# Kernel tuning notes

Hardware: AMD Instinct MI355X
Metric: run time of the kernel (lower is better)

Reference implementation:

```python
import jax, jax.numpy as jnp
import numpy as np

D = 1024  # in_features
H = 16    # head_num

def setup_inputs() -> dict:
    key = jax.random.key(0)
    ks = jax.random.split(key, 11)
    S, B = 2048, 2
    scale = 1.0 / np.sqrt(D)
    inp = {
        'q': jax.random.normal(ks[0], (S, B, D), jnp.float32),
        'k': jax.random.normal(ks[1], (S, B, D), jnp.float32),
        'v': jax.random.normal(ks[2], (S, B, D), jnp.float32),
        'Wq': jax.random.normal(ks[3], (D, D), jnp.float32) * scale,
        'Wk': jax.random.normal(ks[4], (D, D), jnp.float32) * scale,
        'Wv': jax.random.normal(ks[5], (D, D), jnp.float32) * scale,
        'Wo': jax.random.normal(ks[6], (D, D), jnp.float32) * scale,
        'bq': jax.random.normal(ks[7], (D,), jnp.float32) * 0.01,
        'bk': jax.random.normal(ks[8], (D,), jnp.float32) * 0.01,
        'bv': jax.random.normal(ks[9], (D,), jnp.float32) * 0.01,
        'bo': jax.random.normal(ks[10], (D,), jnp.float32) * 0.01,
    }
    return inp

def reference(q, k, v, Wq, Wk, Wv, Wo, bq, bk, bv, bo):
    # q,k,v: (S, B, D) -> (B, S, D)
    q = jnp.transpose(q, (1, 0, 2))
    k = jnp.transpose(k, (1, 0, 2))
    v = jnp.transpose(v, (1, 0, 2))
    # linear + ReLU (torch Linear: x @ W.T + b)
    qh = jax.nn.relu(q @ Wq.T + bq)
    kh = jax.nn.relu(k @ Wk.T + bk)
    vh = jax.nn.relu(v @ Wv.T + bv)
    B, S, _ = qh.shape
    hd = D // H
    # (B, S, H, hd) -> (B, H, S, hd)
    qh = qh.reshape(B, S, H, hd).transpose(0, 2, 1, 3)
    kh = kh.reshape(B, S, H, hd).transpose(0, 2, 1, 3)
    vh = vh.reshape(B, S, H, hd).transpose(0, 2, 1, 3)
    scores = jnp.einsum('bhsd,bhtd->bhst', qh, kh) / np.sqrt(hd).astype(np.float32)
    attn = jax.nn.softmax(scores, axis=-1)
    y = jnp.einsum('bhst,bhtd->bhsd', attn, vh)  # (B, H, S, hd)
    y = y.transpose(0, 2, 1, 3).reshape(B, S, D)
    y = jax.nn.relu(y @ Wo.T + bo)
    return jnp.transpose(y, (1, 0, 2))  # (S, B, D)
```

## Files before the change

kernel.cpp:

```cpp
#include <hip/hip_runtime.h>
#include <stdint.h>

typedef __attribute__((ext_vector_type(8))) short bf8v;
typedef __attribute__((ext_vector_type(4))) float f4v;
typedef __attribute__((ext_vector_type(16))) float f16v;
typedef __attribute__((ext_vector_type(4))) unsigned int u4v;

__device__ __forceinline__ unsigned short f2bf(float f) {
  unsigned int u = __float_as_uint(f);
  u += 0x7fffu + ((u >> 16) & 1u);
  return (unsigned short)(u >> 16);
}

__device__ __forceinline__ float bf2f(unsigned short s) {
  return __uint_as_float((unsigned)s << 16);
}

__device__ __forceinline__ void gload16(const void* g, void* l) {
  __builtin_amdgcn_global_load_lds(
      (__attribute__((address_space(1))) void*)reinterpret_cast<uintptr_t>(g),
      (__attribute__((address_space(3))) void*)reinterpret_cast<uintptr_t>(l),
      16, 0, 0);
}

__device__ __forceinline__ unsigned cvtpk(float lo, float hi) {
  unsigned r;
  asm("v_cvt_pk_bf16_f32 %0, %1, %2" : "=v"(r) : "v"(lo), "v"(hi));
  return r;
}

#define PAIR_SWAP(x, y) asm("v_permlane32_swap_b32 %0, %1" : "+v"(x), "+v"(y))

__global__ __launch_bounds__(256) void cvt_all(
    const float* __restrict__ s0, const float* __restrict__ s1,
    const float* __restrict__ s2, const float* __restrict__ s3,
    const float* __restrict__ s4, const float* __restrict__ s5,
    const float* __restrict__ s6, unsigned short* __restrict__ dst) {
  const size_t NA = (size_t)1 << 22, NW = (size_t)1 << 20;
  size_t i = ((size_t)blockIdx.x * 256 + threadIdx.x) * 8;
  const float* src;
  size_t off;
  if (i < 3 * NA) {
    int a = (int)(i >> 22);
    src = (a == 0) ? s0 : (a == 1) ? s1 : s2;
    off = i & (NA - 1);
  } else {
    size_t j = i - 3 * NA;
    int a = (int)(j >> 20);
    src = (a == 0) ? s3 : (a == 1) ? s4 : (a == 2) ? s5 : s6;
    off = j & (NW - 1);
  }
  const f4v* sp = (const f4v*)(src + off);
  f4v x = sp[0], y = sp[1];
  bf8v r;
  r[0] = (short)f2bf(x[0]); r[1] = (short)f2bf(x[1]);
  r[2] = (short)f2bf(x[2]); r[3] = (short)f2bf(x[3]);
  r[4] = (short)f2bf(y[0]); r[5] = (short)f2bf(y[1]);
  r[6] = (short)f2bf(y[2]); r[7] = (short)f2bf(y[3]);
  *(bf8v*)(dst + i) = r;
}

template <int OMODE, int TN>
__device__ __forceinline__ void gemm_body(
    unsigned short* Al, unsigned short* Bl,
    const unsigned short* __restrict__ A, const unsigned short* __restrict__ W,
    const float* __restrict__ bias, void* __restrict__ out) {
  const int tid = threadIdx.x;
  const int w = tid >> 6, l = tid & 63;
  const int lr = l >> 4, lc = l & 15;
  const int m0 = blockIdx.x * 128, n0 = blockIdx.y * TN;
  const int wr = w >> 1, wc = w & 1;
  const int JW = TN / 32;
  const int BCPW = TN / 64;
  const int BBUF = TN * 32;

  f4v acc[4][JW];
#pragma unroll
  for (int i = 0; i < 4; i++)
#pragma unroll
    for (int j = 0; j < JW; j++) acc[i][j] = (f4v)(0.0f);

  const int NK = 32;
#pragma unroll
  for (int i = 0; i < 2; i++) {
    int chunk = w * 2 + i;
    int e = chunk * 512 + l * 8;
    int r = e >> 5, k = e & 31;
    gload16(A + (size_t)(m0 + r) * 1024 + k, Al + chunk * 512);
  }
#pragma unroll
  for (int i = 0; i < BCPW; i++) {
    int chunk = w * BCPW + i;
    int e = chunk * 512 + l * 8;
    int r = e >> 5, k = e & 31;
    gload16(W + (size_t)(n0 + r) * 1024 + k, Bl + chunk * 512);
  }

  for (int kk = 0; kk < NK; kk++) {
    const int cur = kk & 1;
    __syncthreads();
    if (kk + 1 < NK) {
#pragma unroll
      for (int i = 0; i < 2; i++) {
        int chunk = w * 2 + i;
        int e = chunk * 512 + l * 8;
        int r = e >> 5, k = (kk + 1) * 32 + (e & 31);
        gload16(A + (size_t)(m0 + r) * 1024 + k, Al + (cur ^ 1) * 4096 + chunk * 512);
      }
#pragma unroll
      for (int i = 0; i < BCPW; i++) {
        int chunk = w * BCPW + i;
        int e = chunk * 512 + l * 8;
        int r = e >> 5, k = (kk + 1) * 32 + (e & 31);
        gload16(W + (size_t)(n0 + r) * 1024 + k, Bl + (cur ^ 1) * BBUF + chunk * 512);
      }
    }
    bf8v av[4], bv[JW];
#pragma unroll
    for (int i = 0; i < 4; i++) {
      int row = wr * 64 + i * 16 + lc;
      av[i] = *(const bf8v*)(Al + cur * 4096 + row * 32 + lr * 8);
    }
#pragma unroll
    for (int j = 0; j < JW; j++) {
      int row = wc * (TN / 2) + j * 16 + lc;
      bv[j] = *(const bf8v*)(Bl + cur * BBUF + row * 32 + lr * 8);
    }
#pragma unroll
    for (int i = 0; i < 4; i++)
#pragma unroll
      for (int j = 0; j < JW; j++)
        acc[i][j] = __builtin_amdgcn_mfma_f32_16x16x32_bf16(av[i], bv[j], acc[i][j], 0, 0, 0);
  }

#pragma unroll
  for (int j = 0; j < JW; j++) {
    int n = n0 + wc * (TN / 2) + j * 16 + lc;
    float bj = bias[n];
#pragma unroll
    for (int i = 0; i < 4; i++) {
      int mb = m0 + wr * 64 + i * 16 + lr * 4;
#pragma unroll
      for (int q = 0; q < 4; q++) {
        float val = fmaxf(acc[i][j][q] + bj, 0.0f);
        int m = mb + q;
        if (OMODE == 2) {
          int s = m & 2047, b = m >> 11;
          ((float*)out)[(size_t)(s * 2 + b) * 1024 + n] = val;
        } else {
          int s = m >> 1, b = m & 1;
          int h = n >> 6, d = n & 63;
          if (OMODE == 0)
            ((unsigned short*)out)[((size_t)(b * 16 + h) * 2048 + s) * 64 + d] = f2bf(val);
          else
            ((unsigned short*)out)[((size_t)(b * 16 + h) * 64 + d) * 2048 + s] = f2bf(val);
        }
      }
    }
  }
}

__global__ __launch_bounds__(256) void qkv_gemm(
    const unsigned short* __restrict__ qA, const unsigned short* __restrict__ kA,
    const unsigned short* __restrict__ vA,
    const unsigned short* __restrict__ Wq, const unsigned short* __restrict__ Wk,
    const unsigned short* __restrict__ Wv,
    const float* __restrict__ bq, const float* __restrict__ bk,
    const float* __restrict__ bv,
    unsigned short* __restrict__ Qh, unsigned short* __restrict__ Kh,
    unsigned short* __restrict__ Vt) {
  __shared__ __align__(16) unsigned short Al[2 * 4096];
  __shared__ __align__(16) unsigned short Bl[2 * 4096];
  int z = blockIdx.z;
  if (z == 0)      gemm_body<0, 128>(Al, Bl, qA, Wq, bq, Qh);
  else if (z == 1) gemm_body<0, 128>(Al, Bl, kA, Wk, bk, Kh);
  else             gemm_body<1, 128>(Al, Bl, vA, Wv, bv, Vt);
}

__global__ __launch_bounds__(256) void out_gemm(
    const unsigned short* __restrict__ Y, const unsigned short* __restrict__ Wo,
    const float* __restrict__ bo, float* __restrict__ out) {
  __shared__ __align__(16) unsigned short Al[2 * 4096];
  __shared__ __align__(16) unsigned short Bl[2 * 2048];
  gemm_body<2, 64>(Al, Bl, Y, Wo, bo, out);
}

__global__ __launch_bounds__(256, 2) void attn_kernel(
    const unsigned short* __restrict__ Qh, const unsigned short* __restrict__ Kh,
    const unsigned short* __restrict__ Vt,
    unsigned short* __restrict__ PO, float2* __restrict__ ML) {
  __shared__ __align__(16) unsigned short Kl[2][4096];
  __shared__ __align__(16) unsigned short Vl[2][4096];
  const int tid = threadIdx.x, w = tid >> 6, l = tid & 63;
  const int lo = l & 31, hi = l >> 5;
  const int bh = blockIdx.y;
  const int z = blockIdx.z;
  const int tbeg = z << 10, tend = tbeg + 1024;
  const int q0 = blockIdx.x * 256 + w * 64;
  const size_t qkbase = (size_t)bh * 2048 * 64;
  const size_t vtbase = (size_t)bh * 64 * 2048;
  const float cs = 0.125f * 1.44269504088896341f;

  bf8v qf[2][4];
#pragma unroll
  for (int s = 0; s < 2; s++)
#pragma unroll
    for (int c = 0; c < 4; c++)
      qf[s][c] = *(const bf8v*)(Qh + qkbase + (size_t)(q0 + s * 32 + lo) * 64 + c * 16 + hi * 8);

  f16v oacc[2][2];
  oacc[0][0] = (f16v)(0.0f); oacc[0][1] = (f16v)(0.0f);
  oacc[1][0] = (f16v)(0.0f); oacc[1][1] = (f16v)(0.0f);
  float mrun[2] = {-1e30f, -1e30f};
  float lrun[2] = {0.0f, 0.0f};

  const int swl = (lo & 7) << 4;
  int akb[4], avb[2][2][2];
#pragma unroll
  for (int c = 0; c < 4; c++) akb[c] = lo * 128 + ((c * 32 + hi * 16) ^ swl);
#pragma unroll
  for (int dt = 0; dt < 2; dt++)
#pragma unroll
    for (int kvh = 0; kvh < 2; kvh++)
#pragma unroll
      for (int kc = 0; kc < 2; kc++)
        avb[dt][kvh][kc] = (dt * 32 + lo) * 128 + ((kvh * 64 + kc * 32 + hi * 16) ^ swl);

  int stE[2], stD[2], stKV[2];
#pragma unroll
  for (int i = 0; i < 2; i++) {
    int o = (w * 2 + i) * 1024 + l * 16;
    int row = o >> 7;
    stE[i] = (o ^ ((row & 7) << 4)) >> 1;
    stD[i] = stE[i] >> 6;
    stKV[i] = stE[i] & 63;
  }
  const char* KlB = (const char*)&Kl[0][0];
  const char* VlB = (const char*)&Vl[0][0];

  auto STAGE = [&](int buf, int t0) {
#pragma unroll
    for (int i = 0; i < 2; i++) {
      gload16(Kh + qkbase + (size_t)t0 * 64 + stE[i], (char*)&Kl[buf][0] + (w * 2 + i) * 1024);
      gload16(Vt + vtbase + (size_t)stD[i] * 2048 + t0 + stKV[i], (char*)&Vl[buf][0] + (w * 2 + i) * 1024);
    }
  };

  auto COMPUTE = [&](int bo) {
#pragma unroll
    for (int kvh = 0; kvh < 2; kvh++) {
      bf8v kf[4];
#pragma unroll
      for (int c = 0; c < 4; c++)
        kf[c] = *(const bf8v*)(KlB + bo + kvh * 4096 + akb[c]);
      f16v sa = (f16v)(0.0f), sb = (f16v)(0.0f);
#pragma unroll
      for (int c = 0; c < 4; c++) {
        sa = __builtin_amdgcn_mfma_f32_32x32x16_bf16(kf[c], qf[0][c], sa, 0, 0, 0);
        sb = __builtin_amdgcn_mfma_f32_32x32x16_bf16(kf[c], qf[1][c], sb, 0, 0, 0);
      }
      bf8v vf[2][2];
#pragma unroll
      for (int dt = 0; dt < 2; dt++)
#pragma unroll
        for (int kc = 0; kc < 2; kc++)
          vf[dt][kc] = *(const bf8v*)(VlB + bo + avb[dt][kvh][kc]);

#pragma unroll
      for (int s = 0; s < 2; s++) {
        const f16v& sc16 = (s == 0) ? sa : sb;
        float t0 = fmaxf(fmaxf(sc16[0], sc16[1]), sc16[2]);
        float t1 = fmaxf(fmaxf(sc16[3], sc16[4]), sc16[5]);
        float t2 = fmaxf(fmaxf(sc16[6], sc16[7]), sc16[8]);
        float t3 = fmaxf(fmaxf(sc16[9], sc16[10]), sc16[11]);
        float t4 = fmaxf(fmaxf(sc16[12], sc16[13]), sc16[14]);
        float lm = fmaxf(fmaxf(fmaxf(t0, t1), fmaxf(t2, t3)), fmaxf(t4, sc16[15]));
        float msc = lm * cs;
        if (!__all(msc <= mrun[s] + 8.0f)) {
          float x = msc, y = msc;
          PAIR_SWAP(x, y);
          float pm = fmaxf(x, y);
          float mnew = fmaxf(mrun[s], pm);
          float scl = __builtin_amdgcn_exp2f(mrun[s] - mnew);
          lrun[s] *= scl;
#pragma unroll
          for (int dt = 0; dt < 2; dt++)
#pragma unroll
            for (int r = 0; r < 16; r++) oacc[s][dt][r] *= scl;
          mrun[s] = mnew;
        }
        float p[16];
#pragma unroll
        for (int r = 0; r < 16; r++)
          p[r] = __builtin_amdgcn_exp2f(sc16[r] * cs - mrun[s]);
        float s01 = (p[0] + p[1]) + (p[2] + p[3]);
        float s23 = (p[4] + p[5]) + (p[6] + p[7]);
        float s45 = (p[8] + p[9]) + (p[10] + p[11]);
        float s67 = (p[12] + p[13]) + (p[14] + p[15]);
        lrun[s] += (s01 + s23) + (s45 + s67);
        bf8v pf[2];
#pragma unroll
        for (int kc = 0; kc < 2; kc++) {
          unsigned a0 = cvtpk(p[kc * 8 + 0], p[kc * 8 + 1]);
          unsigned a1 = cvtpk(p[kc * 8 + 2], p[kc * 8 + 3]);
          unsigned b0 = cvtpk(p[kc * 8 + 4], p[kc * 8 + 5]);
          unsigned b1 = cvtpk(p[kc * 8 + 6], p[kc * 8 + 7]);
          PAIR_SWAP(a0, b0);
          PAIR_SWAP(a1, b1);
          u4v pw;
          pw[0] = a0; pw[1] = a1; pw[2] = b0; pw[3] = b1;
          pf[kc] = __builtin_bit_cast(bf8v, pw);
        }
#pragma unroll
        for (int dt = 0; dt < 2; dt++)
#pragma unroll
          for (int kc = 0; kc < 2; kc++)
            oacc[s][dt] = __builtin_amdgcn_mfma_f32_32x32x16_bf16(vf[dt][kc], pf[kc],
                                                                 oacc[s][dt], 0, 0, 0);
      }
    }
  };

  STAGE(0, tbeg);
  __syncthreads();
#pragma unroll 1
  for (int t0 = tbeg; t0 < tend; t0 += 128) {
    STAGE(1, t0 + 64);
    COMPUTE(0);
    __syncthreads();
    if (t0 + 128 < tend) STAGE(0, t0 + 128);
    COMPUTE(8192);
    __syncthreads();
  }

#pragma unroll
  for (int s = 0; s < 2; s++) {
    float x = lrun[s], y = lrun[s];
    PAIR_SWAP(x, y);
    float lt = x + y;
    int q = q0 + s * 32 + lo;
    size_t prow = (size_t)(z * 32 + bh) * 2048 + q;
    if (hi == 0) ML[prow] = float2{mrun[s], lt};
    unsigned short* pp = PO + prow * 64;
#pragma unroll
    for (int dt = 0; dt < 2; dt++)
#pragma unroll
      for (int r = 0; r < 16; r++) {
        int d = dt * 32 + (r & 3) + 8 * (r >> 2) + 4 * hi;
        pp[d] = f2bf(oacc[s][dt][r]);
      }
  }
}

__global__ __launch_bounds__(256) void combine_kernel(
    const unsigned short* __restrict__ PO, const float2* __restrict__ ML,
    unsigned short* __restrict__ Y) {
  int idx = blockIdx.x * 256 + threadIdx.x;
  int row = idx >> 1, hr = idx & 1;
  int bh = row >> 11, q = row & 2047;
  float2 ml0 = ML[row], ml1 = ML[65536 + row];
  float M = fmaxf(ml0.x, ml1.x);
  float a0 = __builtin_amdgcn_exp2f(ml0.x - M);
  float a1 = __builtin_amdgcn_exp2f(ml1.x - M);
  float L = ml0.y * a0 + ml1.y * a1;
  float s0 = a0 / L, s1 = a1 / L;
  const unsigned short* p0 = PO + (size_t)row * 64 + hr * 32;
  const unsigned short* p1 = PO + ((size_t)65536 + row) * 64 + hr * 32;
  int b = bh >> 4, h = bh & 15;
  unsigned short* yp = Y + (((size_t)(b * 2048 + q)) << 10) + h * 64 + hr * 32;
#pragma unroll
  for (int g = 0; g < 4; g++) {
    bf8v v0 = *(const bf8v*)(p0 + g * 8);
    bf8v v1 = *(const bf8v*)(p1 + g * 8);
    bf8v r;
#pragma unroll
    for (int j = 0; j < 8; j++)
      r[j] = (short)f2bf(bf2f((unsigned short)v0[j]) * s0 +
                         bf2f((unsigned short)v1[j]) * s1);
    *(bf8v*)(yp + g * 8) = r;
  }
}

extern "C" void kernel_launch(void* const* d_in, const int* in_sizes, int n_in,
                              void* d_out, int out_size, void* d_ws, size_t ws_size,
                              hipStream_t stream) {
  const float* q  = (const float*)d_in[0];
  const float* k  = (const float*)d_in[1];
  const float* v  = (const float*)d_in[2];
  const float* Wq = (const float*)d_in[3];
  const float* Wk = (const float*)d_in[4];
  const float* Wv = (const float*)d_in[5];
  const float* Wo = (const float*)d_in[6];
  const float* bq = (const float*)d_in[7];
  const float* bk = (const float*)d_in[8];
  const float* bv = (const float*)d_in[9];
  const float* bo = (const float*)d_in[10];

  const size_t NA = (size_t)4096 * 1024;
  const size_t NW = (size_t)1024 * 1024;
  unsigned short* qA  = (unsigned short*)d_ws;
  unsigned short* kA  = qA  + NA;
  unsigned short* vA  = kA  + NA;
  unsigned short* WqB = vA  + NA;
  unsigned short* WkB = WqB + NW;
  unsigned short* WvB = WkB + NW;
  unsigned short* WoB = WvB + NW;
  unsigned short* Qh  = WoB + NW;
  unsigned short* Kh  = Qh  + NA;
  unsigned short* Vt  = Kh  + NA;
  unsigned short* Y   = Vt  + NA;

  unsigned short* PO = qA;
  float2*         ML = (float2*)vA;

  cvt_all<<<dim3(8192), 256, 0, stream>>>(q, k, v, Wq, Wk, Wv, Wo, qA);

  qkv_gemm<<<dim3(32, 8, 3), 256, 0, stream>>>(qA, kA, vA, WqB, WkB, WvB,
                                               bq, bk, bv, Qh, Kh, Vt);
  attn_kernel<<<dim3(8, 32, 2), 256, 0, stream>>>(Qh, Kh, Vt, PO, ML);
  combine_kernel<<<dim3(512), 256, 0, stream>>>(PO, ML, Y);
  out_gemm<<<dim3(32, 16), 256, 0, stream>>>(Y, WoB, bo, (float*)d_out);
}
```

Measured before the change: 127.7 us.

## Fuse fp32 activation conversion into QKV GEMM, tune attention priorities and partials

The standalone pass that converts the q/k/v activations to bf16 is removed. The QKV GEMM now loads fp32 activation tiles directly into LDS (swizzled) and packs them to bf16 in registers before the MFMAs, which drops a full read-write pass over the activations. The attention kernel also gains s_setprio around its MFMA blocks, a tighter rescale threshold (5 instead of 8), and per-split normalization with fp16 partial outputs, and the combine step is adjusted to match. In exchange, the GEMM moves twice as many bytes per A tile through LDS, and using fp16 for the partials adds some precision risk.

```diff
diff --git a/kernel.cpp b/kernel.cpp
--- a/kernel.cpp
+++ b/kernel.cpp
@@ -12,8 +12,13 @@
   return (unsigned short)(u >> 16);
 }
 
-__device__ __forceinline__ float bf2f(unsigned short s) {
-  return __uint_as_float((unsigned)s << 16);
+__device__ __forceinline__ unsigned short f2h(float f) {
+  _Float16 h = (_Float16)f;
+  return __builtin_bit_cast(unsigned short, h);
+}
+
+__device__ __forceinline__ float h2f(unsigned short s) {
+  return (float)__builtin_bit_cast(_Float16, s);
 }
 
 __device__ __forceinline__ void gload16(const void* g, void* l) {
@@ -31,25 +36,15 @@
 
 #define PAIR_SWAP(x, y) asm("v_permlane32_swap_b32 %0, %1" : "+v"(x), "+v"(y))
 
-__global__ __launch_bounds__(256) void cvt_all(
+__global__ __launch_bounds__(256) void cvt_w(
     const float* __restrict__ s0, const float* __restrict__ s1,
     const float* __restrict__ s2, const float* __restrict__ s3,
-    const float* __restrict__ s4, const float* __restrict__ s5,
-    const float* __restrict__ s6, unsigned short* __restrict__ dst) {
-  const size_t NA = (size_t)1 << 22, NW = (size_t)1 << 20;
+    unsigned short* __restrict__ dst) {
+  const size_t NW = (size_t)1 << 20;
   size_t i = ((size_t)blockIdx.x * 256 + threadIdx.x) * 8;
-  const float* src;
-  size_t off;
-  if (i < 3 * NA) {
-    int a = (int)(i >> 22);
-    src = (a == 0) ? s0 : (a == 1) ? s1 : s2;
-    off = i & (NA - 1);
-  } else {
-    size_t j = i - 3 * NA;
-    int a = (int)(j >> 20);
-    src = (a == 0) ? s3 : (a == 1) ? s4 : (a == 2) ? s5 : s6;
-    off = j & (NW - 1);
-  }
+  int a = (int)(i >> 20);
+  const float* src = (a == 0) ? s0 : (a == 1) ? s1 : (a == 2) ? s2 : s3;
+  size_t off = i & (NW - 1);
   const f4v* sp = (const f4v*)(src + off);
   f4v x = sp[0], y = sp[1];
   bf8v r;
@@ -60,11 +55,129 @@
   *(bf8v*)(dst + i) = r;
 }
 
-template <int OMODE, int TN>
-__device__ __forceinline__ void gemm_body(
+template <int OMODE>
+__device__ __forceinline__ void gemmA32_body(
+    float* Al, unsigned short* Bl,
+    const float* __restrict__ A, const unsigned short* __restrict__ W,
+    const float* __restrict__ bias, unsigned short* __restrict__ out) {
+  const int tid = threadIdx.x;
+  const int w = tid >> 6, l = tid & 63;
+  const int lr = l >> 4, lc = l & 15;
+  const int m0 = blockIdx.x * 128, n0 = blockIdx.y * 128;
+  const int wr = w >> 1, wc = w & 1;
+
+  f4v acc[4][4];
+#pragma unroll
+  for (int i = 0; i < 4; i++)
+#pragma unroll
+    for (int j = 0; j < 4; j++) acc[i][j] = (f4v)(0.0f);
+
+  int aR[4], aK[4];
+#pragma unroll
+  for (int i = 0; i < 4; i++) {
+    int o = (w * 4 + i) * 1024 + l * 16;
+    int row = o >> 7;
+    int e = (o ^ ((row & 7) << 4)) >> 2;
+    aR[i] = e >> 5; aK[i] = e & 31;
+  }
+
+  const int NK = 32;
+#pragma unroll
+  for (int i = 0; i < 4; i++)
+    gload16(A + (size_t)(m0 + aR[i]) * 1024 + aK[i], (char*)Al + (w * 4 + i) * 1024);
+#pragma unroll
+  for (int i = 0; i < 2; i++) {
+    int chunk = w * 2 + i;
+    int e = chunk * 512 + l * 8;
+    int r = e >> 5, k = e & 31;
+    gload16(W + (size_t)(n0 + r) * 1024 + k, Bl + chunk * 512);
+  }
+
+  for (int kk = 0; kk < NK; kk++) {
+    const int cur = kk & 1;
+    __syncthreads();
+    if (kk + 1 < NK) {
+#pragma unroll
+      for (int i = 0; i < 4; i++)
+        gload16(A + (size_t)(m0 + aR[i]) * 1024 + (kk + 1) * 32 + aK[i],
+                (char*)Al + (cur ^ 1) * 16384 + (w * 4 + i) * 1024);
+#pragma unroll
+      for (int i = 0; i < 2; i++) {
+        int chunk = w * 2 + i;
+        int e = chunk * 512 + l * 8;
+        int r = e >> 5, k = (kk + 1) * 32 + (e & 31);
+        gload16(W + (size_t)(n0 + r) * 1024 + k, Bl + (cur ^ 1) * 4096 + chunk * 512);
+      }
+    }
+    const char* AlB = (const char*)Al + cur * 16384;
+    bf8v av[4], bv[4];
+#pragma unroll
+    for (int i = 0; i < 4; i++) {
+      int row = wr * 64 + i * 16 + lc;
+      int b0 = (row * 128 + lr * 32) ^ ((row & 7) << 4);
+      f4v x = *(const f4v*)(AlB + b0);
+      f4v y = *(const f4v*)(AlB + (b0 ^ 16));
+      u4v aw;
+      aw[0] = cvtpk(x[0], x[1]); aw[1] = cvtpk(x[2], x[3]);
+      aw[2] = cvtpk(y[0], y[1]); aw[3] = cvtpk(y[2], y[3]);
+      av[i] = __builtin_bit_cast(bf8v, aw);
+    }
+#pragma unroll
+    for (int j = 0; j < 4; j++) {
+      int row = wc * 64 + j * 16 + lc;
+      bv[j] = *(const bf8v*)(Bl + cur * 4096 + row * 32 + lr * 8);
+    }
+#pragma unroll
+    for (int i = 0; i < 4; i++)
+#pragma unroll
+      for (int j = 0; j < 4; j++)
+        acc[i][j] = __builtin_amdgcn_mfma_f32_16x16x32_bf16(av[i], bv[j], acc[i][j], 0, 0, 0);
+  }
+
+#pragma unroll
+  for (int j = 0; j < 4; j++) {
+    int n = n0 + wc * 64 + j * 16 + lc;
+    float bj = bias[n];
+#pragma unroll
+    for (int i = 0; i < 4; i++) {
+      int mb = m0 + wr * 64 + i * 16 + lr * 4;
+#pragma unroll
+      for (int q = 0; q < 4; q++) {
+        float val = fmaxf(acc[i][j][q] + bj, 0.0f);
+        int m = mb + q;
+        int s = m >> 1, b = m & 1;
+        int h = n >> 6, d = n & 63;
+        if (OMODE == 0)
+          out[((size_t)(b * 16 + h) * 2048 + s) * 64 + d] = f2bf(val);
+        else
+          out[((size_t)(b * 16 + h) * 64 + d) * 2048 + s] = f2bf(val);
+      }
+    }
+  }
+}
+
+__global__ __launch_bounds__(256) void qkv_gemm(
+    const float* __restrict__ qA, const float* __restrict__ kA,
+    const float* __restrict__ vA,
+    const unsigned short* __restrict__ Wq, const unsigned short* __restrict__ Wk,
+    const unsigned short* __restrict__ Wv,
+    const float* __restrict__ bq, const float* __restrict__ bk,
+    const float* __restrict__ bv,
+    unsigned short* __restrict__ Qh, unsigned short* __restrict__ Kh,
+    unsigned short* __restrict__ Vt) {
+  __shared__ __align__(16) float Al[2 * 4096];
+  __shared__ __align__(16) unsigned short Bl[2 * 4096];
+  int z = blockIdx.z;
+  if (z == 0)      gemmA32_body<0>(Al, Bl, qA, Wq, bq, Qh);
+  else if (z == 1) gemmA32_body<0>(Al, Bl, kA, Wk, bk, Kh);
+  else             gemmA32_body<1>(Al, Bl, vA, Wv, bv, Vt);
+}
+
+template <int TN>
+__device__ __forceinline__ void gemm_body2(
     unsigned short* Al, unsigned short* Bl,
     const unsigned short* __restrict__ A, const unsigned short* __restrict__ W,
-    const float* __restrict__ bias, void* __restrict__ out) {
+    const float* __restrict__ bias, float* __restrict__ out) {
   const int tid = threadIdx.x;
   const int w = tid >> 6, l = tid & 63;
   const int lr = l >> 4, lc = l & 15;
@@ -144,37 +257,11 @@
       for (int q = 0; q < 4; q++) {
         float val = fmaxf(acc[i][j][q] + bj, 0.0f);
         int m = mb + q;
-        if (OMODE == 2) {
-          int s = m & 2047, b = m >> 11;
-          ((float*)out)[(size_t)(s * 2 + b) * 1024 + n] = val;
-        } else {
-          int s = m >> 1, b = m & 1;
-          int h = n >> 6, d = n & 63;
-          if (OMODE == 0)
-            ((unsigned short*)out)[((size_t)(b * 16 + h) * 2048 + s) * 64 + d] = f2bf(val);
-          else
-            ((unsigned short*)out)[((size_t)(b * 16 + h) * 64 + d) * 2048 + s] = f2bf(val);
-        }
-      }
-    }
-  }
-}
-
-__global__ __launch_bounds__(256) void qkv_gemm(
-    const unsigned short* __restrict__ qA, const unsigned short* __restrict__ kA,
-    const unsigned short* __restrict__ vA,
-    const unsigned short* __restrict__ Wq, const unsigned short* __restrict__ Wk,
-    const unsigned short* __restrict__ Wv,
-    const float* __restrict__ bq, const float* __restrict__ bk,
-    const float* __restrict__ bv,
-    unsigned short* __restrict__ Qh, unsigned short* __restrict__ Kh,
-    unsigned short* __restrict__ Vt) {
-  __shared__ __align__(16) unsigned short Al[2 * 4096];
-  __shared__ __align__(16) unsigned short Bl[2 * 4096];
-  int z = blockIdx.z;
-  if (z == 0)      gemm_body<0, 128>(Al, Bl, qA, Wq, bq, Qh);
-  else if (z == 1) gemm_body<0, 128>(Al, Bl, kA, Wk, bk, Kh);
-  else             gemm_body<1, 128>(Al, Bl, vA, Wv, bv, Vt);
+        int s = m & 2047, b = m >> 11;
+        out[(size_t)(s * 2 + b) * 1024 + n] = val;
+      }
+    }
+  }
 }
 
 __global__ __launch_bounds__(256) void out_gemm(
@@ -182,20 +269,20 @@
     const float* __restrict__ bo, float* __restrict__ out) {
   __shared__ __align__(16) unsigned short Al[2 * 4096];
   __shared__ __align__(16) unsigned short Bl[2 * 2048];
-  gemm_body<2, 64>(Al, Bl, Y, Wo, bo, out);
+  gemm_body2<64>(Al, Bl, Y, Wo, bo, out);
 }
 
 __global__ __launch_bounds__(256, 2) void attn_kernel(
     const unsigned short* __restrict__ Qh, const unsigned short* __restrict__ Kh,
     const unsigned short* __restrict__ Vt,
-    unsigned short* __restrict__ PO, float2* __restrict__ ML) {
+    unsigned short* __restrict__ PO, float2* __restrict__ ML, int kvlen) {
   __shared__ __align__(16) unsigned short Kl[2][4096];
   __shared__ __align__(16) unsigned short Vl[2][4096];
   const int tid = threadIdx.x, w = tid >> 6, l = tid & 63;
   const int lo = l & 31, hi = l >> 5;
   const int bh = blockIdx.y;
   const int z = blockIdx.z;
-  const int tbeg = z << 10, tend = tbeg + 1024;
+  const int tbeg = z * kvlen, tend = tbeg + kvlen;
   const int q0 = blockIdx.x * 256 + w * 64;
   const size_t qkbase = (size_t)bh * 2048 * 64;
   const size_t vtbase = (size_t)bh * 64 * 2048;
@@ -254,11 +341,13 @@
       for (int c = 0; c < 4; c++)
         kf[c] = *(const bf8v*)(KlB + bo + kvh * 4096 + akb[c]);
       f16v sa = (f16v)(0.0f), sb = (f16v)(0.0f);
+      __builtin_amdgcn_s_setprio(1);
 #pragma unroll
       for (int c = 0; c < 4; c++) {
         sa = __builtin_amdgcn_mfma_f32_32x32x16_bf16(kf[c], qf[0][c], sa, 0, 0, 0);
         sb = __builtin_amdgcn_mfma_f32_32x32x16_bf16(kf[c], qf[1][c], sb, 0, 0, 0);
       }
+      __builtin_amdgcn_s_setprio(0);
       bf8v vf[2][2];
 #pragma unroll
       for (int dt = 0; dt < 2; dt++)
@@ -276,7 +365,7 @@
         float t4 = fmaxf(fmaxf(sc16[12], sc16[13]), sc16[14]);
         float lm = fmaxf(fmaxf(fmaxf(t0, t1), fmaxf(t2, t3)), fmaxf(t4, sc16[15]));
         float msc = lm * cs;
-        if (!__all(msc <= mrun[s] + 8.0f)) {
+        if (!__all(msc <= mrun[s] + 5.0f)) {
           float x = msc, y = msc;
           PAIR_SWAP(x, y);
           float pm = fmaxf(x, y);
@@ -311,12 +400,14 @@
           pw[0] = a0; pw[1] = a1; pw[2] = b0; pw[3] = b1;
           pf[kc] = __builtin_bit_cast(bf8v, pw);
         }
+        __builtin_amdgcn_s_setprio(1);
 #pragma unroll
         for (int dt = 0; dt < 2; dt++)
 #pragma unroll
           for (int kc = 0; kc < 2; kc++)
             oacc[s][dt] = __builtin_amdgcn_mfma_f32_32x32x16_bf16(vf[dt][kc], pf[kc],
                                                                  oacc[s][dt], 0, 0, 0);
+        __builtin_amdgcn_s_setprio(0);
       }
     }
   };
@@ -338,6 +429,7 @@
     float x = lrun[s], y = lrun[s];
     PAIR_SWAP(x, y);
     float lt = x + y;
+    float inv = 1.0f / lt;
     int q = q0 + s * 32 + lo;
     size_t prow = (size_t)(z * 32 + bh) * 2048 + q;
     if (hi == 0) ML[prow] = float2{mrun[s], lt};
@@ -347,7 +439,7 @@
 #pragma unroll
       for (int r = 0; r < 16; r++) {
         int d = dt * 32 + (r & 3) + 8 * (r >> 2) + 4 * hi;
-        pp[d] = f2bf(oacc[s][dt][r]);
+        pp[d] = f2h(oacc[s][dt][r] * inv);
       }
   }
 }
@@ -360,14 +452,14 @@
   int bh = row >> 11, q = row & 2047;
   float2 ml0 = ML[row], ml1 = ML[65536 + row];
   float M = fmaxf(ml0.x, ml1.x);
-  float a0 = __builtin_amdgcn_exp2f(ml0.x - M);
-  float a1 = __builtin_amdgcn_exp2f(ml1.x - M);
-  float L = ml0.y * a0 + ml1.y * a1;
-  float s0 = a0 / L, s1 = a1 / L;
+  float w0 = ml0.y * __builtin_amdgcn_exp2f(ml0.x - M);
+  float w1 = ml1.y * __builtin_amdgcn_exp2f(ml1.x - M);
+  float invW = 1.0f / (w0 + w1);
+  w0 *= invW; w1 *= invW;
+  int b = bh >> 4, h = bh & 15;
+  unsigned short* yp = Y + (((size_t)(b * 2048 + q)) << 10) + h * 64 + hr * 32;
   const unsigned short* p0 = PO + (size_t)row * 64 + hr * 32;
   const unsigned short* p1 = PO + ((size_t)65536 + row) * 64 + hr * 32;
-  int b = bh >> 4, h = bh & 15;
-  unsigned short* yp = Y + (((size_t)(b * 2048 + q)) << 10) + h * 64 + hr * 32;
 #pragma unroll
   for (int g = 0; g < 4; g++) {
     bf8v v0 = *(const bf8v*)(p0 + g * 8);
@@ -375,8 +467,8 @@
     bf8v r;
 #pragma unroll
     for (int j = 0; j < 8; j++)
-      r[j] = (short)f2bf(bf2f((unsigned short)v0[j]) * s0 +
-                         bf2f((unsigned short)v1[j]) * s1);
+      r[j] = (short)f2bf(h2f((unsigned short)v0[j]) * w0 +
+                         h2f((unsigned short)v1[j]) * w1);
     *(bf8v*)(yp + g * 8) = r;
   }
 }
@@ -398,10 +490,7 @@
 
   const size_t NA = (size_t)4096 * 1024;
   const size_t NW = (size_t)1024 * 1024;
-  unsigned short* qA  = (unsigned short*)d_ws;
-  unsigned short* kA  = qA  + NA;
-  unsigned short* vA  = kA  + NA;
-  unsigned short* WqB = vA  + NA;
+  unsigned short* WqB = (unsigned short*)d_ws;
   unsigned short* WkB = WqB + NW;
   unsigned short* WvB = WkB + NW;
   unsigned short* WoB = WvB + NW;
@@ -409,15 +498,14 @@
   unsigned short* Kh  = Qh  + NA;
   unsigned short* Vt  = Kh  + NA;
   unsigned short* Y   = Vt  + NA;
-
-  unsigned short* PO = qA;
-  float2*         ML = (float2*)vA;
-
-  cvt_all<<<dim3(8192), 256, 0, stream>>>(q, k, v, Wq, Wk, Wv, Wo, qA);
-
-  qkv_gemm<<<dim3(32, 8, 3), 256, 0, stream>>>(qA, kA, vA, WqB, WkB, WvB,
+  unsigned short* PO  = Y   + NA;
+  float2*         ML  = (float2*)(PO + 2 * NA);
+
+  cvt_w<<<dim3(2048), 256, 0, stream>>>(Wq, Wk, Wv, Wo, WqB);
+
+  qkv_gemm<<<dim3(32, 8, 3), 256, 0, stream>>>(q, k, v, WqB, WkB, WvB,
                                                bq, bk, bv, Qh, Kh, Vt);
-  attn_kernel<<<dim3(8, 32, 2), 256, 0, stream>>>(Qh, Kh, Vt, PO, ML);
+  attn_kernel<<<dim3(8, 32, 2), 256, 0, stream>>>(Qh, Kh, Vt, PO, ML, 1024);
   combine_kernel<<<dim3(512), 256, 0, stream>>>(PO, ML, Y);
   out_gemm<<<dim3(32, 16), 256, 0, stream>>>(Y, WoB, bo, (float*)d_out);
 }
```

After: 127.5 us. Within noise of the previous version (-0.1%).

## Shrink QKV GEMM tile, add MFMA priority hints, store fp16 normalized partials

Applied to the files above, without the earlier changes.

The QKV GEMM tile width drops from 128 to 64, doubling the grid so more blocks are available to fill the GPU. In attention, s_setprio raises wave priority around the MFMA sections, and the lazy-rescale threshold is tightened from 8 to 5. Partial outputs are now normalized by their row sum and stored as fp16 rather than bf16, and the combine step is adjusted to match. The KV split length becomes a runtime parameter. Together these mix occupancy tuning, scheduling hints and a precision change, and the smaller GEMM tile lowers per-block data reuse.

```diff
diff --git a/kernel.cpp b/kernel.cpp
--- a/kernel.cpp
+++ b/kernel.cpp
@@ -12,8 +12,13 @@
   return (unsigned short)(u >> 16);
 }
 
-__device__ __forceinline__ float bf2f(unsigned short s) {
-  return __uint_as_float((unsigned)s << 16);
+__device__ __forceinline__ unsigned short f2h(float f) {
+  _Float16 h = (_Float16)f;
+  return __builtin_bit_cast(unsigned short, h);
+}
+
+__device__ __forceinline__ float h2f(unsigned short s) {
+  return (float)__builtin_bit_cast(_Float16, s);
 }
 
 __device__ __forceinline__ void gload16(const void* g, void* l) {
@@ -170,11 +175,11 @@
     unsigned short* __restrict__ Qh, unsigned short* __restrict__ Kh,
     unsigned short* __restrict__ Vt) {
   __shared__ __align__(16) unsigned short Al[2 * 4096];
-  __shared__ __align__(16) unsigned short Bl[2 * 4096];
+  __shared__ __align__(16) unsigned short Bl[2 * 2048];
   int z = blockIdx.z;
-  if (z == 0)      gemm_body<0, 128>(Al, Bl, qA, Wq, bq, Qh);
-  else if (z == 1) gemm_body<0, 128>(Al, Bl, kA, Wk, bk, Kh);
-  else             gemm_body<1, 128>(Al, Bl, vA, Wv, bv, Vt);
+  if (z == 0)      gemm_body<0, 64>(Al, Bl, qA, Wq, bq, Qh);
+  else if (z == 1) gemm_body<0, 64>(Al, Bl, kA, Wk, bk, Kh);
+  else             gemm_body<1, 64>(Al, Bl, vA, Wv, bv, Vt);
 }
 
 __global__ __launch_bounds__(256) void out_gemm(
@@ -188,14 +193,14 @@
 __global__ __launch_bounds__(256, 2) void attn_kernel(
     const unsigned short* __restrict__ Qh, const unsigned short* __restrict__ Kh,
     const unsigned short* __restrict__ Vt,
-    unsigned short* __restrict__ PO, float2* __restrict__ ML) {
+    unsigned short* __restrict__ PO, float2* __restrict__ ML, int kvlen) {
   __shared__ __align__(16) unsigned short Kl[2][4096];
   __shared__ __align__(16) unsigned short Vl[2][4096];
   const int tid = threadIdx.x, w = tid >> 6, l = tid & 63;
   const int lo = l & 31, hi = l >> 5;
   const int bh = blockIdx.y;
   const int z = blockIdx.z;
-  const int tbeg = z << 10, tend = tbeg + 1024;
+  const int tbeg = z * kvlen, tend = tbeg + kvlen;
   const int q0 = blockIdx.x * 256 + w * 64;
   const size_t qkbase = (size_t)bh * 2048 * 64;
   const size_t vtbase = (size_t)bh * 64 * 2048;
@@ -254,11 +259,13 @@
       for (int c = 0; c < 4; c++)
         kf[c] = *(const bf8v*)(KlB + bo + kvh * 4096 + akb[c]);
       f16v sa = (f16v)(0.0f), sb = (f16v)(0.0f);
+      __builtin_amdgcn_s_setprio(1);
 #pragma unroll
       for (int c = 0; c < 4; c++) {
         sa = __builtin_amdgcn_mfma_f32_32x32x16_bf16(kf[c], qf[0][c], sa, 0, 0, 0);
         sb = __builtin_amdgcn_mfma_f32_32x32x16_bf16(kf[c], qf[1][c], sb, 0, 0, 0);
       }
+      __builtin_amdgcn_s_setprio(0);
       bf8v vf[2][2];
 #pragma unroll
       for (int dt = 0; dt < 2; dt++)
@@ -276,7 +283,7 @@
         float t4 = fmaxf(fmaxf(sc16[12], sc16[13]), sc16[14]);
         float lm = fmaxf(fmaxf(fmaxf(t0, t1), fmaxf(t2, t3)), fmaxf(t4, sc16[15]));
         float msc = lm * cs;
-        if (!__all(msc <= mrun[s] + 8.0f)) {
+        if (!__all(msc <= mrun[s] + 5.0f)) {
           float x = msc, y = msc;
           PAIR_SWAP(x, y);
           float pm = fmaxf(x, y);
@@ -311,12 +318,14 @@
           pw[0] = a0; pw[1] = a1; pw[2] = b0; pw[3] = b1;
           pf[kc] = __builtin_bit_cast(bf8v, pw);
         }
+        __builtin_amdgcn_s_setprio(1);
 #pragma unroll
         for (int dt = 0; dt < 2; dt++)
 #pragma unroll
           for (int kc = 0; kc < 2; kc++)
             oacc[s][dt] = __builtin_amdgcn_mfma_f32_32x32x16_bf16(vf[dt][kc], pf[kc],
                                                                  oacc[s][dt], 0, 0, 0);
+        __builtin_amdgcn_s_setprio(0);
       }
     }
   };
@@ -338,6 +347,7 @@
     float x = lrun[s], y = lrun[s];
     PAIR_SWAP(x, y);
     float lt = x + y;
+    float inv = 1.0f / lt;
     int q = q0 + s * 32 + lo;
     size_t prow = (size_t)(z * 32 + bh) * 2048 + q;
     if (hi == 0) ML[prow] = float2{mrun[s], lt};
@@ -347,7 +357,7 @@
 #pragma unroll
       for (int r = 0; r < 16; r++) {
         int d = dt * 32 + (r & 3) + 8 * (r >> 2) + 4 * hi;
-        pp[d] = f2bf(oacc[s][dt][r]);
+        pp[d] = f2h(oacc[s][dt][r] * inv);
       }
   }
 }
@@ -360,14 +370,14 @@
   int bh = row >> 11, q = row & 2047;
   float2 ml0 = ML[row], ml1 = ML[65536 + row];
   float M = fmaxf(ml0.x, ml1.x);
-  float a0 = __builtin_amdgcn_exp2f(ml0.x - M);
-  float a1 = __builtin_amdgcn_exp2f(ml1.x - M);
-  float L = ml0.y * a0 + ml1.y * a1;
-  float s0 = a0 / L, s1 = a1 / L;
+  float w0 = ml0.y * __builtin_amdgcn_exp2f(ml0.x - M);
+  float w1 = ml1.y * __builtin_amdgcn_exp2f(ml1.x - M);
+  float invW = 1.0f / (w0 + w1);
+  w0 *= invW; w1 *= invW;
+  int b = bh >> 4, h = bh & 15;
+  unsigned short* yp = Y + (((size_t)(b * 2048 + q)) << 10) + h * 64 + hr * 32;
   const unsigned short* p0 = PO + (size_t)row * 64 + hr * 32;
   const unsigned short* p1 = PO + ((size_t)65536 + row) * 64 + hr * 32;
-  int b = bh >> 4, h = bh & 15;
-  unsigned short* yp = Y + (((size_t)(b * 2048 + q)) << 10) + h * 64 + hr * 32;
 #pragma unroll
   for (int g = 0; g < 4; g++) {
     bf8v v0 = *(const bf8v*)(p0 + g * 8);
@@ -375,8 +385,8 @@
     bf8v r;
 #pragma unroll
     for (int j = 0; j < 8; j++)
-      r[j] = (short)f2bf(bf2f((unsigned short)v0[j]) * s0 +
-                         bf2f((unsigned short)v1[j]) * s1);
+      r[j] = (short)f2bf(h2f((unsigned short)v0[j]) * w0 +
+                         h2f((unsigned short)v1[j]) * w1);
     *(bf8v*)(yp + g * 8) = r;
   }
 }
@@ -415,9 +425,9 @@
 
   cvt_all<<<dim3(8192), 256, 0, stream>>>(q, k, v, Wq, Wk, Wv, Wo, qA);
 
-  qkv_gemm<<<dim3(32, 8, 3), 256, 0, stream>>>(qA, kA, vA, WqB, WkB, WvB,
-                                               bq, bk, bv, Qh, Kh, Vt);
-  attn_kernel<<<dim3(8, 32, 2), 256, 0, stream>>>(Qh, Kh, Vt, PO, ML);
+  qkv_gemm<<<dim3(32, 16, 3), 256, 0, stream>>>(qA, kA, vA, WqB, WkB, WvB,
+                                                bq, bk, bv, Qh, Kh, Vt);
+  attn_kernel<<<dim3(8, 32, 2), 256, 0, stream>>>(Qh, Kh, Vt, PO, ML, 1024);
   combine_kernel<<<dim3(512), 256, 0, stream>>>(PO, ML, Y);
   out_gemm<<<dim3(32, 16), 256, 0, stream>>>(Y, WoB, bo, (float*)d_out);
 }
```

Measured after the change: 139.4 us. 9.2% more time.
